# Optimization experiments

Hardware: AMD Instinct MI355X
Metric: run time of the kernel (lower is better)

## Reference

```python
import jax, jax.numpy as jnp
import numpy as np

B, S, F, H = 4, 1024, 512, 16
D = F // H  # head_dim = 32

def setup_inputs() -> dict:
    key = jax.random.key(0)
    ks = jax.random.split(key, 9)
    init = lambda k, shp: 0.1 * jax.random.normal(k, shp, dtype=jnp.float32)
    return {
        "kv": jax.random.normal(ks[0], (B, S, F), dtype=jnp.float32),
        "q": jax.random.normal(ks[1], (B, S, F), dtype=jnp.float32),
        "mask": jnp.ones((B, 1, S, S), dtype=jnp.int32),
        "Wq": init(ks[2], (F, F)),
        "Wk": init(ks[3], (F, F)),
        "Wv": init(ks[4], (F, F)),
        "Wo": init(ks[5], (F, F)),
        "rel_table": init(ks[6], (2 * S + 1, D)),  # nn.Embed(2*length_q+1, head_dim)
        "Wrel": init(ks[7], (D, D)),  # rel_pos_dense, no bias
    }

def reference(kv, q, mask, Wq, Wk, Wv, Wo, rel_table, Wrel):
    b, s, f = q.shape
    h, d = H, f // H
    qh = (q @ Wq).reshape(b, s, h, d)
    kh = (kv @ Wk).reshape(b, s, h, d)
    vh = (kv @ Wv).reshape(b, s, h, d)
    # raw content scores [b,h,q,k]
    scores = jnp.einsum('bqhd,bkhd->bhqk', qh, kh)
    # relative-position embedding: dist in [0, 2s], table lookup + dense
    dist = jnp.arange(s)[None, :] - jnp.arange(s)[:, None] + s  # [q,k]
    emb = rel_table[dist] @ Wrel  # [q,k,d]
    scores = scores + jnp.einsum('bqhd,qkd->bhqk', qh, emb)
    scores = scores / jnp.sqrt(jnp.asarray(d, scores.dtype))
    # mask-select before softmax (mask [b,1,q,k] broadcast over heads)
    scores = jnp.where(mask > 0, scores, -jnp.inf)
    attn = jax.nn.softmax(scores, axis=-1)
    out = jnp.einsum('bhqk,bkhd->bqhd', attn, vh).reshape(b, s, f)
    return out @ Wo  # dropout is identity (training=False)
```

## Files before the change

### kernel.cpp

```cpp
#include <hip/hip_runtime.h>

#define S_ 1024
#define H_ 16
#define D_ 32

typedef float f32x4 __attribute__((ext_vector_type(4)));
typedef short bf16x8 __attribute__((ext_vector_type(8)));
typedef unsigned long long u64;

static __device__ __forceinline__ short f2b(float f) {
    union { float f; unsigned u; } x; x.f = f;
    unsigned u = x.u;
    unsigned r = u + 0x7fffu + ((u >> 16) & 1u);
    return (short)(r >> 16);
}
static __device__ __forceinline__ unsigned pk_rne(float lo, float hi) {
    union { float f; unsigned u; } a, b; a.f = lo; b.f = hi;
    unsigned ul = a.u + 0x7fffu + ((a.u >> 16) & 1u);
    unsigned uh = b.u + 0x7fffu + ((b.u >> 16) & 1u);
    return __builtin_amdgcn_perm(uh, ul, 0x07060302u);
}
static __device__ __forceinline__ unsigned pk_trunc(float lo, float hi) {
    union { float f; unsigned u; } a, b; a.f = lo; b.f = hi;
    return __builtin_amdgcn_perm(b.u, a.u, 0x07060302u);
}
static __device__ __forceinline__ float bperm(int bidx, float v) {
    union { float f; int i; } x; x.f = v;
    x.i = __builtin_amdgcn_ds_bpermute(bidx, x.i);
    return x.f;
}
static __device__ __forceinline__ int stg(int row, int c8) {
    return row * 40 + (c8 ^ ((row & 3) << 3));
}
static __device__ __forceinline__ int stg64(int row, int c8) {
    return row * 72 + (c8 ^ ((row & 3) << 3));
}

__global__ __launch_bounds__(256)
void prep_kernel(const float* __restrict__ rt, short* __restrict__ relb,
                 const int* __restrict__ mask, u64* __restrict__ mbits,
                 const float* __restrict__ Wq, const float* __restrict__ Wk,
                 const float* __restrict__ Wv, const float* __restrict__ Wo,
                 short* __restrict__ Wt)
{
    __shared__ float ls[32][33];
    int bid = blockIdx.x, t = threadIdx.x;
    if (bid < 257) {
        int i = bid * 256 + t;
        if (i < 2049 * 32) relb[i] = f2b(rt[i]);
        return;
    }
    bid -= 257;
    if (bid < 4096) {
        #pragma unroll
        for (int j = 0; j < 4; ++j) {
            int i = bid * 1024 + j * 256 + t;
            u64 bal = __ballot(mask[i] > 0);
            if ((t & 63) == 0) mbits[i >> 6] = bal;
        }
        return;
    }
    bid -= 4096;
    int mat = bid >> 8, tl = bid & 255, ti = tl >> 4, tj = tl & 15;
    const float* W = (mat == 0) ? Wq : (mat == 1) ? Wk : (mat == 2) ? Wv : Wo;
    int r = t >> 3, c = (t & 7) * 4;
    float4 v = *(const float4*)(W + (long)(ti * 32 + r) * 512 + tj * 32 + c);
    ls[r][c] = v.x; ls[r][c + 1] = v.y; ls[r][c + 2] = v.z; ls[r][c + 3] = v.w;
    __syncthreads();
    int nl = t >> 3, kk = (t & 7) * 4;
    uint2 o = { pk_rne(ls[kk][nl], ls[kk + 1][nl]),
                pk_rne(ls[kk + 2][nl], ls[kk + 3][nl]) };
    *(uint2*)(Wt + ((long)mat * 512 + tj * 32 + nl) * 512 + ti * 32 + kk) = o;
}

__global__ __launch_bounds__(256)
void gemm3_kernel(const float* __restrict__ q, const float* __restrict__ kv,
                  const short* __restrict__ Wt,
                  short* __restrict__ qh, short* __restrict__ kh, short* __restrict__ vt,
                  float scale)
{
    __shared__ __align__(16) short a_s[64 * 72];
    __shared__ __align__(16) short b_s[64 * 72];
    const int t = threadIdx.x;
    const int w = t >> 6, lane = t & 63, l15 = lane & 15, quad = lane >> 4;
    const int wm = w & 1, wn = w >> 1;

    int bid = blockIdx.x;
    const int mat = bid >> 9;
    const int rr_ = bid & 511;
    const int bm = (rr_ >> 3) * 64, bn = (rr_ & 7) * 64;
    const float* A = (mat == 0) ? q : kv;
    const short* Wm = Wt + (long)mat * 262144;

    const int srow = t >> 2, scg = (t & 3) << 4;
    f32x4 acc[2][2] = {};

    for (int k0 = 0; k0 < 512; k0 += 64) {
        {
            const float* ap = A + (long)(bm + srow) * 512 + k0 + scg;
            float4 v0 = *(const float4*)(ap);
            float4 v1 = *(const float4*)(ap + 4);
            float4 v2 = *(const float4*)(ap + 8);
            float4 v3 = *(const float4*)(ap + 12);
            uint4 o0 = { pk_rne(v0.x, v0.y), pk_rne(v0.z, v0.w),
                         pk_rne(v1.x, v1.y), pk_rne(v1.z, v1.w) };
            uint4 o1 = { pk_rne(v2.x, v2.y), pk_rne(v2.z, v2.w),
                         pk_rne(v3.x, v3.y), pk_rne(v3.z, v3.w) };
            *(uint4*)(a_s + stg64(srow, scg)) = o0;
            *(uint4*)(a_s + stg64(srow, scg + 8)) = o1;
        }
        {
            const short* bp = Wm + (long)(bn + srow) * 512 + k0 + scg;
            *(bf16x8*)(b_s + stg64(srow, scg))     = *(const bf16x8*)(bp);
            *(bf16x8*)(b_s + stg64(srow, scg + 8)) = *(const bf16x8*)(bp + 8);
        }
        __syncthreads();
        bf16x8 af[2][2], bfr[2][2];
        #pragma unroll
        for (int i = 0; i < 2; ++i)
            #pragma unroll
            for (int ks = 0; ks < 2; ++ks) {
                af[i][ks]  = *(const bf16x8*)(a_s + stg64(wm * 32 + i * 16 + l15, ks * 32 + quad * 8));
                bfr[i][ks] = *(const bf16x8*)(b_s + stg64(wn * 32 + i * 16 + l15, ks * 32 + quad * 8));
            }
        if (mat == 2) {
            #pragma unroll
            for (int i = 0; i < 2; ++i)
                #pragma unroll
                for (int j = 0; j < 2; ++j)
                    #pragma unroll
                    for (int ks = 0; ks < 2; ++ks)
                        acc[i][j] = __builtin_amdgcn_mfma_f32_16x16x32_bf16(bfr[i][ks], af[j][ks], acc[i][j], 0, 0, 0);
        } else {
            #pragma unroll
            for (int i = 0; i < 2; ++i)
                #pragma unroll
                for (int j = 0; j < 2; ++j)
                    #pragma unroll
                    for (int ks = 0; ks < 2; ++ks)
                        acc[i][j] = __builtin_amdgcn_mfma_f32_16x16x32_bf16(af[i][ks], bfr[j][ks], acc[i][j], 0, 0, 0);
        }
        __syncthreads();
    }

    if (mat < 2) {
        short* out = (mat == 0) ? qh : kh;
        float alpha = (mat == 0) ? scale : 1.0f;
        #pragma unroll
        for (int i = 0; i < 2; ++i)
            #pragma unroll
            for (int j = 0; j < 2; ++j)
                #pragma unroll
                for (int r = 0; r < 4; ++r) {
                    int m = bm + wm * 32 + i * 16 + quad * 4 + r;
                    int n = bn + wn * 32 + j * 16 + l15;
                    int bb = m >> 10, s = m & 1023, hh = n >> 5, dd = n & 31;
                    out[((long)((bb * 16 + hh) * 1024 + s)) * 32 + dd] = f2b(acc[i][j][r] * alpha);
                }
    } else {
        #pragma unroll
        for (int i = 0; i < 2; ++i)
            #pragma unroll
            for (int j = 0; j < 2; ++j)
                #pragma unroll
                for (int r = 0; r < 4; ++r) {
                    int n = bn + wn * 32 + i * 16 + quad * 4 + r;
                    int m = bm + wm * 32 + j * 16 + l15;
                    int bb = m >> 10, s = m & 1023, hh = n >> 5, dd = n & 31;
                    int sp = (s & ~63) | ((s & 15) << 2) | ((s >> 4) & 3);
                    vt[((long)((bb * 16 + hh) * 32 + dd)) * 1024 + sp] = f2b(acc[i][j][r]);
                }
    }
}

__global__ __launch_bounds__(256)
void gemm_out_kernel(const short* __restrict__ ao, const short* __restrict__ Wt,
                     float* __restrict__ out)
{
    __shared__ __align__(16) short a_s[64 * 72];
    __shared__ __align__(16) short b_s[64 * 72];
    const int t = threadIdx.x;
    const int w = t >> 6, lane = t & 63, l15 = lane & 15, quad = lane >> 4;
    const int wm = w & 1, wn = w >> 1;
    const int bm = (blockIdx.x >> 3) * 64, bn = (blockIdx.x & 7) * 64;
    const short* Wm = Wt + (long)3 * 262144;
    const int srow = t >> 2, scg = (t & 3) << 4;
    f32x4 acc[2][2] = {};

    for (int k0 = 0; k0 < 512; k0 += 64) {
        {
            const short* apb = ao + (long)(bm + srow) * 512 + k0 + scg;
            *(bf16x8*)(a_s + stg64(srow, scg))     = *(const bf16x8*)(apb);
            *(bf16x8*)(a_s + stg64(srow, scg + 8)) = *(const bf16x8*)(apb + 8);
            const short* bpb = Wm + (long)(bn + srow) * 512 + k0 + scg;
            *(bf16x8*)(b_s + stg64(srow, scg))     = *(const bf16x8*)(bpb);
            *(bf16x8*)(b_s + stg64(srow, scg + 8)) = *(const bf16x8*)(bpb + 8);
        }
        __syncthreads();
        bf16x8 af[2][2], bfr[2][2];
        #pragma unroll
        for (int i = 0; i < 2; ++i)
            #pragma unroll
            for (int ks = 0; ks < 2; ++ks) {
                af[i][ks]  = *(const bf16x8*)(a_s + stg64(wm * 32 + i * 16 + l15, ks * 32 + quad * 8));
                bfr[i][ks] = *(const bf16x8*)(b_s + stg64(wn * 32 + i * 16 + l15, ks * 32 + quad * 8));
            }
        #pragma unroll
        for (int i = 0; i < 2; ++i)
            #pragma unroll
            for (int j = 0; j < 2; ++j)
                #pragma unroll
                for (int ks = 0; ks < 2; ++ks)
                    acc[i][j] = __builtin_amdgcn_mfma_f32_16x16x32_bf16(af[i][ks], bfr[j][ks], acc[i][j], 0, 0, 0);
        __syncthreads();
    }
    #pragma unroll
    for (int i = 0; i < 2; ++i)
        #pragma unroll
        for (int j = 0; j < 2; ++j)
            #pragma unroll
            for (int r = 0; r < 4; ++r) {
                int m = bm + wm * 32 + i * 16 + quad * 4 + r;
                int n = bn + wn * 32 + j * 16 + l15;
                out[(long)m * 512 + n] = acc[i][j][r];
            }
}

__global__ __launch_bounds__(256, 4)
void attn_kernel(const short* __restrict__ qh, const float* __restrict__ wrel,
                 const short* __restrict__ kh, const short* __restrict__ vt,
                 const short* __restrict__ relb, const u64* __restrict__ mbits,
                 short* __restrict__ ao)
{
    __shared__ __align__(16) short smem[4 * 2 * 16 * 72];
    const int t = threadIdx.x;
    const int w = t >> 6, lane = t & 63, l15 = lane & 15, quad = lane >> 4;
    short* pw0 = smem + w * (2 * 16 * 72);
    short* pw1 = pw0 + 16 * 72;

    const int gw = blockIdx.x * 4 + w;
    const int qt = gw & 63, h = (gw >> 6) & 15, b = gw >> 10;
    const int q0 = qt * 16, bh = b * H_ + h;

    const long qbase = ((long)bh * S_ + q0 + l15) * D_ + quad * 8;
    const bf16x8 a_qh = *(const bf16x8*)(qh + qbase);
    const long kv_bh = (long)bh * S_ * D_;
    const u64* mrow = mbits + ((long)b * S_ + q0 + quad * 4) * 16;

    bf16x8 a_qr;
    {
        #pragma unroll
        for (int nt = 0; nt < 2; ++nt) {
            const float* wp = wrel + (long)(nt * 16 + l15) * 32 + quad * 8;
            float4 w0 = *(const float4*)(wp);
            float4 w1 = *(const float4*)(wp + 4);
            bf16x8 bw;
            *(uint4*)&bw = (uint4){ pk_rne(w0.x, w0.y), pk_rne(w0.z, w0.w),
                                    pk_rne(w1.x, w1.y), pk_rne(w1.z, w1.w) };
            f32x4 z = {0.f, 0.f, 0.f, 0.f};
            f32x4 cq = __builtin_amdgcn_mfma_f32_16x16x32_bf16(a_qh, bw, z, 0, 0, 0);
            #pragma unroll
            for (int r = 0; r < 4; ++r)
                pw0[(quad * 4 + r) * 36 + nt * 16 + l15] = f2b(cq[r]);
        }
        asm volatile("" ::: "memory");
        a_qr = *(const bf16x8*)(pw0 + l15 * 36 + quad * 8);
        asm volatile("" ::: "memory");
    }

    int bidx[4]; int cnd[4];
    #pragma unroll
    for (int r = 0; r < 4; ++r) {
        int qq = quad * 4 + r;
        bidx[r] = (quad * 16 + ((l15 + 15 - qq) & 15)) * 4;
        cnd[r] = (l15 > qq);
    }

    f32x4 oacc[2] = {};
    float l4[4] = {0.f, 0.f, 0.f, 0.f};

    bf16x8 preg0 = {}, preg1 = {};
    bf16x8 bv00 = {}, bv01 = {}, bv10 = {}, bv11 = {};

    bf16x8 kf[4], rf[5];
    {
        const int ub0 = -q0 + (S_ - 15);
        #pragma unroll
        for (int ut = 0; ut < 5; ++ut)
            rf[ut] = *(const bf16x8*)(relb + (long)(ub0 + ut * 16 + l15) * D_ + quad * 8);
        #pragma unroll
        for (int kt = 0; kt < 4; ++kt)
            kf[kt] = *(const bf16x8*)(kh + kv_bh + (long)(kt * 16 + l15) * D_ + quad * 8);
    }

    for (int c = 0; c < 16; ++c) {
        const int kbase = c * 64;
        short* pwbuf = (c & 1) ? pw1 : pw0;

        f32x4 ctf[5], sc[4];
        #pragma unroll
        for (int ut = 0; ut < 5; ++ut) {
            f32x4 z = {0.f, 0.f, 0.f, 0.f};
            ctf[ut] = __builtin_amdgcn_mfma_f32_16x16x32_bf16(a_qr, rf[ut], z, 0, 0, 0);
        }
        #pragma unroll
        for (int kt = 0; kt < 4; ++kt) {
            f32x4 z = {0.f, 0.f, 0.f, 0.f};
            sc[kt] = __builtin_amdgcn_mfma_f32_16x16x32_bf16(a_qh, kf[kt], z, 0, 0, 0);
        }
        if (c) {
            oacc[0] = __builtin_amdgcn_mfma_f32_16x16x32_bf16(preg0, bv00, oacc[0], 0, 0, 0);
            oacc[1] = __builtin_amdgcn_mfma_f32_16x16x32_bf16(preg0, bv01, oacc[1], 0, 0, 0);
            oacc[0] = __builtin_amdgcn_mfma_f32_16x16x32_bf16(preg1, bv10, oacc[0], 0, 0, 0);
            oacc[1] = __builtin_amdgcn_mfma_f32_16x16x32_bf16(preg1, bv11, oacc[1], 0, 0, 0);
        }
        {
            const int cn = (c < 15) ? c + 1 : 15;
            const int kbn = cn * 64, ubn = kbn - q0 + (S_ - 15);
            #pragma unroll
            for (int ut = 0; ut < 5; ++ut)
                rf[ut] = *(const bf16x8*)(relb + (long)(ubn + ut * 16 + l15) * D_ + quad * 8);
            #pragma unroll
            for (int kt = 0; kt < 4; ++kt)
                kf[kt] = *(const bf16x8*)(kh + kv_bh + (long)(kbn + kt * 16 + l15) * D_ + quad * 8);
        }
        bv00 = *(const bf16x8*)(vt + kv_bh + (long)(l15) * S_ + kbase + quad * 8);
        bv01 = *(const bf16x8*)(vt + kv_bh + (long)(16 + l15) * S_ + kbase + quad * 8);
        bv10 = *(const bf16x8*)(vt + kv_bh + (long)(l15) * S_ + kbase + 32 + quad * 8);
        bv11 = *(const bf16x8*)(vt + kv_bh + (long)(16 + l15) * S_ + kbase + 32 + quad * 8);

        #pragma unroll
        for (int r = 0; r < 4; ++r) {
            float tt[5];
            #pragma unroll
            for (int ut = 0; ut < 5; ++ut) tt[ut] = bperm(bidx[r], ctf[ut][r]);
            float s0 = sc[0][r] + (cnd[r] ? tt[1] : tt[0]);
            float s1 = sc[1][r] + (cnd[r] ? tt[2] : tt[1]);
            float s2 = sc[2][r] + (cnd[r] ? tt[3] : tt[2]);
            float s3 = sc[3][r] + (cnd[r] ? tt[4] : tt[3]);
            u64 mw = mrow[r * 16 + c] >> l15;
            unsigned lo = (unsigned)mw, hi = (unsigned)(mw >> 32);
            float p0 = __expf(s0); p0 = (lo & 1u)         ? p0 : 0.f;
            float p1 = __expf(s1); p1 = ((lo >> 16) & 1u) ? p1 : 0.f;
            float p2 = __expf(s2); p2 = (hi & 1u)         ? p2 : 0.f;
            float p3 = __expf(s3); p3 = ((hi >> 16) & 1u) ? p3 : 0.f;
            l4[r] += (p0 + p1) + (p2 + p3);
            u64 pv = ((u64)pk_trunc(p2, p3) << 32) | (u64)pk_trunc(p0, p1);
            *(u64*)(pwbuf + (quad * 4 + r) * 72 + l15 * 4) = pv;
        }
        asm volatile("" ::: "memory");
        preg0 = *(const bf16x8*)(pwbuf + l15 * 72 + quad * 8);
        preg1 = *(const bf16x8*)(pwbuf + l15 * 72 + 32 + quad * 8);
    }
    oacc[0] = __builtin_amdgcn_mfma_f32_16x16x32_bf16(preg0, bv00, oacc[0], 0, 0, 0);
    oacc[1] = __builtin_amdgcn_mfma_f32_16x16x32_bf16(preg0, bv01, oacc[1], 0, 0, 0);
    oacc[0] = __builtin_amdgcn_mfma_f32_16x16x32_bf16(preg1, bv10, oacc[0], 0, 0, 0);
    oacc[1] = __builtin_amdgcn_mfma_f32_16x16x32_bf16(preg1, bv11, oacc[1], 0, 0, 0);

    #pragma unroll
    for (int r = 0; r < 4; ++r) {
        float l = l4[r];
        l += __shfl_xor(l, 1, 64);
        l += __shfl_xor(l, 2, 64);
        l += __shfl_xor(l, 4, 64);
        l += __shfl_xor(l, 8, 64);
        float inv = 1.0f / l;
        int row = q0 + quad * 4 + r;
        #pragma unroll
        for (int dt = 0; dt < 2; ++dt)
            ao[((long)(b * S_ + row) * H_ + h) * D_ + dt * 16 + l15] = f2b(oacc[dt][r] * inv);
    }
}

extern "C" void kernel_launch(void* const* d_in, const int* in_sizes, int n_in,
                              void* d_out, int out_size, void* d_ws, size_t ws_size,
                              hipStream_t stream) {
    (void)in_sizes; (void)n_in; (void)out_size; (void)ws_size;
    const float* kv   = (const float*)d_in[0];
    const float* q    = (const float*)d_in[1];
    const int*   mask = (const int*)d_in[2];
    const float* Wq   = (const float*)d_in[3];
    const float* Wk   = (const float*)d_in[4];
    const float* Wv   = (const float*)d_in[5];
    const float* Wo   = (const float*)d_in[6];
    const float* rt   = (const float*)d_in[7];
    const float* Wrel = (const float*)d_in[8];

    char* ws = (char*)d_ws;
    short* qh   = (short*)(ws);
    short* kh   = (short*)(ws + (4u  << 20));
    short* vt   = (short*)(ws + (8u  << 20));
    short* ao   = (short*)(ws + (12u << 20));
    short* Wt   = (short*)(ws + (16u << 20));
    short* relb = (short*)(ws + (18u << 20));
    u64*  mbits = (u64*) (ws + (18u << 20) + (256u << 10));

    const float scale = 0.17677669529663687f;

    prep_kernel<<<257 + 4096 + 1024, 256, 0, stream>>>(
        rt, relb, mask, mbits, Wq, Wk, Wv, Wo, Wt);

    gemm3_kernel<<<1536, 256, 0, stream>>>(q, kv, Wt, qh, kh, vt, scale);

    attn_kernel<<<1024, 256, 0, stream>>>(qh, Wrel, kh, vt, relb, mbits, ao);

    gemm_out_kernel<<<512, 256, 0, stream>>>(ao, Wt, (float*)d_out);
}
```

Baseline: 202.5 us.

## Split attention key range across two waves per query tile and merge via LDS

Each 16-row query tile is now handled by two waves, each covering half of the key chunks (8 of 16). The waves then combine partial outputs and row sums through shared memory after a block barrier, and the grid is doubled. Mask words are also prefetched one chunk ahead into registers, and the chunk loop is fully unrolled. This shortens the serial per-wave loop and adds parallelism, at the cost of a cross-wave reduction, a __syncthreads, and duplicated per-wave setup such as the Q·Wrel projection.

New measurement: 282.5 us. +39.5%, slower.

```diff
diff --git a/kernel.cpp b/kernel.cpp
--- a/kernel.cpp
+++ b/kernel.cpp
@@ -28,9 +28,6 @@
     union { float f; int i; } x; x.f = v;
     x.i = __builtin_amdgcn_ds_bpermute(bidx, x.i);
     return x.f;
-}
-static __device__ __forceinline__ int stg(int row, int c8) {
-    return row * 40 + (c8 ^ ((row & 3) << 3));
 }
 static __device__ __forceinline__ int stg64(int row, int c8) {
     return row * 72 + (c8 ^ ((row & 3) << 3));
@@ -238,9 +235,11 @@
     short* pw0 = smem + w * (2 * 16 * 72);
     short* pw1 = pw0 + 16 * 72;
 
-    const int gw = blockIdx.x * 4 + w;
+    const int half = w & 1, qsel = w >> 1;
+    const int gw = blockIdx.x * 2 + qsel;
     const int qt = gw & 63, h = (gw >> 6) & 15, b = gw >> 10;
     const int q0 = qt * 16, bh = b * H_ + h;
+    const int c0 = half * 8;
 
     const long qbase = ((long)bh * S_ + q0 + l15) * D_ + quad * 8;
     const bf16x8 a_qh = *(const bf16x8*)(qh + qbase);
@@ -283,19 +282,24 @@
     bf16x8 bv00 = {}, bv01 = {}, bv10 = {}, bv11 = {};
 
     bf16x8 kf[4], rf[5];
+    u64 mcur[4];
     {
-        const int ub0 = -q0 + (S_ - 15);
+        const int ub0 = c0 * 64 - q0 + (S_ - 15);
         #pragma unroll
         for (int ut = 0; ut < 5; ++ut)
             rf[ut] = *(const bf16x8*)(relb + (long)(ub0 + ut * 16 + l15) * D_ + quad * 8);
         #pragma unroll
         for (int kt = 0; kt < 4; ++kt)
-            kf[kt] = *(const bf16x8*)(kh + kv_bh + (long)(kt * 16 + l15) * D_ + quad * 8);
-    }
-
-    for (int c = 0; c < 16; ++c) {
+            kf[kt] = *(const bf16x8*)(kh + kv_bh + (long)(c0 * 64 + kt * 16 + l15) * D_ + quad * 8);
+        #pragma unroll
+        for (int r = 0; r < 4; ++r) mcur[r] = mrow[r * 16 + c0];
+    }
+
+    #pragma unroll
+    for (int i = 0; i < 8; ++i) {
+        const int c = c0 + i;
         const int kbase = c * 64;
-        short* pwbuf = (c & 1) ? pw1 : pw0;
+        short* pwbuf = (i & 1) ? pw1 : pw0;
 
         f32x4 ctf[5], sc[4];
         #pragma unroll
@@ -308,21 +312,23 @@
             f32x4 z = {0.f, 0.f, 0.f, 0.f};
             sc[kt] = __builtin_amdgcn_mfma_f32_16x16x32_bf16(a_qh, kf[kt], z, 0, 0, 0);
         }
-        if (c) {
+        if (i) {
             oacc[0] = __builtin_amdgcn_mfma_f32_16x16x32_bf16(preg0, bv00, oacc[0], 0, 0, 0);
             oacc[1] = __builtin_amdgcn_mfma_f32_16x16x32_bf16(preg0, bv01, oacc[1], 0, 0, 0);
             oacc[0] = __builtin_amdgcn_mfma_f32_16x16x32_bf16(preg1, bv10, oacc[0], 0, 0, 0);
             oacc[1] = __builtin_amdgcn_mfma_f32_16x16x32_bf16(preg1, bv11, oacc[1], 0, 0, 0);
         }
-        {
-            const int cn = (c < 15) ? c + 1 : 15;
-            const int kbn = cn * 64, ubn = kbn - q0 + (S_ - 15);
+        u64 mnext[4];
+        if (i < 7) {
+            const int kbn = kbase + 64, ubn = kbn - q0 + (S_ - 15);
             #pragma unroll
             for (int ut = 0; ut < 5; ++ut)
                 rf[ut] = *(const bf16x8*)(relb + (long)(ubn + ut * 16 + l15) * D_ + quad * 8);
             #pragma unroll
             for (int kt = 0; kt < 4; ++kt)
                 kf[kt] = *(const bf16x8*)(kh + kv_bh + (long)(kbn + kt * 16 + l15) * D_ + quad * 8);
+            #pragma unroll
+            for (int r = 0; r < 4; ++r) mnext[r] = mrow[r * 16 + c + 1];
         }
         bv00 = *(const bf16x8*)(vt + kv_bh + (long)(l15) * S_ + kbase + quad * 8);
         bv01 = *(const bf16x8*)(vt + kv_bh + (long)(16 + l15) * S_ + kbase + quad * 8);
@@ -338,7 +344,7 @@
             float s1 = sc[1][r] + (cnd[r] ? tt[2] : tt[1]);
             float s2 = sc[2][r] + (cnd[r] ? tt[3] : tt[2]);
             float s3 = sc[3][r] + (cnd[r] ? tt[4] : tt[3]);
-            u64 mw = mrow[r * 16 + c] >> l15;
+            u64 mw = mcur[r] >> l15;
             unsigned lo = (unsigned)mw, hi = (unsigned)(mw >> 32);
             float p0 = __expf(s0); p0 = (lo & 1u)         ? p0 : 0.f;
             float p1 = __expf(s1); p1 = ((lo >> 16) & 1u) ? p1 : 0.f;
@@ -351,6 +357,10 @@
         asm volatile("" ::: "memory");
         preg0 = *(const bf16x8*)(pwbuf + l15 * 72 + quad * 8);
         preg1 = *(const bf16x8*)(pwbuf + l15 * 72 + 32 + quad * 8);
+        if (i < 7) {
+            #pragma unroll
+            for (int r = 0; r < 4; ++r) mcur[r] = mnext[r];
+        }
     }
     oacc[0] = __builtin_amdgcn_mfma_f32_16x16x32_bf16(preg0, bv00, oacc[0], 0, 0, 0);
     oacc[1] = __builtin_amdgcn_mfma_f32_16x16x32_bf16(preg0, bv01, oacc[1], 0, 0, 0);
@@ -364,11 +374,33 @@
         l += __shfl_xor(l, 2, 64);
         l += __shfl_xor(l, 4, 64);
         l += __shfl_xor(l, 8, 64);
-        float inv = 1.0f / l;
-        int row = q0 + quad * 4 + r;
+        l4[r] = l;
+    }
+
+    asm volatile("" ::: "memory");
+    float* fo = (float*)pw0;
+    float* fl = (float*)pw1;
+    #pragma unroll
+    for (int r = 0; r < 4; ++r) {
         #pragma unroll
         for (int dt = 0; dt < 2; ++dt)
-            ao[((long)(b * S_ + row) * H_ + h) * D_ + dt * 16 + l15] = f2b(oacc[dt][r] * inv);
+            fo[(quad * 4 + r) * 32 + dt * 16 + l15] = oacc[dt][r];
+        if (l15 == 0) fl[quad * 4 + r] = l4[r];
+    }
+    __syncthreads();
+    if (half == 0) {
+        const float* po = (const float*)(smem + (w ^ 1) * (2 * 16 * 72));
+        const float* pl = po + 16 * 72 / 2;
+        #pragma unroll
+        for (int r = 0; r < 4; ++r) {
+            int row = quad * 4 + r;
+            float inv = 1.0f / (l4[r] + pl[row]);
+            #pragma unroll
+            for (int dt = 0; dt < 2; ++dt) {
+                float o = oacc[dt][r] + po[row * 32 + dt * 16 + l15];
+                ao[((long)(b * S_ + q0 + row) * H_ + h) * D_ + dt * 16 + l15] = f2b(o * inv);
+            }
+        }
     }
 }
 
@@ -402,7 +434,7 @@
 
     gemm3_kernel<<<1536, 256, 0, stream>>>(q, kv, Wt, qh, kh, vt, scale);
 
-    attn_kernel<<<1024, 256, 0, stream>>>(qh, Wrel, kh, vt, relb, mbits, ao);
+    attn_kernel<<<2048, 256, 0, stream>>>(qh, Wrel, kh, vt, relb, mbits, ao);
 
     gemm_out_kernel<<<512, 256, 0, stream>>>(ao, Wt, (float*)d_out);
 }
```
